# Kernel optimization log

Measured on AMD Instinct MI355X. Metric: run time of the kernel, lower is better.

Reference implementation:

```python
import jax, jax.numpy as jnp
import numpy as np

N = 131072      # total nodes (1024 graphs x 128 nodes)
G = 1024        # graphs in batch
NPG = 128       # nodes per graph (power of 2 -> clean Haar halving)
H = 128         # hidden = out channels
DEG = 16        # avg degree
E = N * DEG     # edges
L = 3           # num_layers
C = 10          # num_classes
BN_EPS = 1e-5
INV_SQRT2 = 0.7071067811865476  # Haar low-pass normalization


def setup_inputs() -> dict:
    key = jax.random.key(0)
    ks = jax.random.split(key, 8)
    x = jax.random.normal(ks[0], (N, H), jnp.float32)
    # within-graph random edges: per-edge graph offset + local endpoint
    offs = (jnp.arange(E, dtype=jnp.int32) // (NPG * DEG)) * NPG
    src = jax.random.randint(ks[1], (E,), 0, NPG, jnp.int32) + offs
    dst = jax.random.randint(ks[2], (E,), 0, NPG, jnp.int32) + offs
    edge_index = jnp.stack([src, dst])
    w = lambda k, s: jax.random.normal(k, s, jnp.float32) * 0.05
    return dict(
        x=x, edge_index=edge_index,
        lin_start_w=w(ks[3], (H, H)), lin_start_b=jnp.zeros((H,), jnp.float32),
        bn_start_g=jnp.ones((H,), jnp.float32), bn_start_b=jnp.zeros((H,), jnp.float32),
        conv_w1=w(ks[4], (L, H, H)), conv_b1=jnp.zeros((L, H), jnp.float32),
        conv_bn_g=jnp.ones((L, H), jnp.float32), conv_bn_b=jnp.zeros((L, H), jnp.float32),
        conv_w2=w(ks[5], (L, H, H)), conv_b2=jnp.zeros((L, H), jnp.float32),
        bn_g=jnp.ones((L, H), jnp.float32), bn_b=jnp.zeros((L, H), jnp.float32),
        bne_g=jnp.ones((L, H), jnp.float32), bne_b=jnp.zeros((L, H), jnp.float32),
        lin_w=w(ks[6], (L * H, C)), lin_b=jnp.zeros((C,), jnp.float32),
    )


def _bn(x, g, b):
    # training-mode BatchNorm1d: batch stats, biased variance
    m = x.mean(0)
    v = x.var(0)
    return (x - m) * jax.lax.rsqrt(v + BN_EPS) * g + b


def reference(x, edge_index, lin_start_w, lin_start_b, bn_start_g, bn_start_b,
              conv_w1, conv_b1, conv_bn_g, conv_bn_b, conv_w2, conv_b2,
              bn_g, bn_b, bne_g, bne_b, lin_w, lin_b):
    n = N
    ei = edge_index
    # lin_before_conv stage
    x = jax.nn.relu(_bn(x @ lin_start_w + lin_start_b, bn_start_g, bn_start_b))
    embds = []
    for i in range(L):
        # GINConv (eps=0): mlp(x + sum_{j->i} x_j)
        agg = jax.ops.segment_sum(x[ei[0]], ei[1], num_segments=n)
        h = x + agg
        h = h @ conv_w1[i] + conv_b1[i]
        h = jax.nn.relu(_bn(h, conv_bn_g[i], conv_bn_b[i]))
        h = h @ conv_w2[i] + conv_b2[i]
        x = jax.nn.relu(_bn(h, bn_g[i], bn_b[i]))
        # Haar pooling: pairwise low-pass coarsening, (x_{2k}+x_{2k+1})/sqrt(2)
        n = n // 2
        cluster = jnp.arange(2 * n, dtype=jnp.int32) // 2
        x = jax.ops.segment_sum(x, cluster, num_segments=n) * INV_SQRT2
        ei = ei // 2  # coarsen edge endpoints to cluster ids
        npg = NPG >> (i + 1)  # nodes per graph after pooling
        batch = jnp.arange(n, dtype=jnp.int32) // npg
        # global_add_pool + BN (dropout in eval mode -> identity)
        embd = jax.ops.segment_sum(x, batch, num_segments=G)
        embd = jax.nn.relu(_bn(embd, bne_g[i], bne_b[i]))
        embds.append(embd)
    return jnp.concatenate(embds, axis=-1) @ lin_w + lin_b  # [G, C]
```

## Files before the change

### kernel.cpp

```cpp
#include <hip/hip_runtime.h>

#define N_NODES  131072
#define G_GRAPHS 1024
#define NPG0     128
#define HDIM     128
#define E_EDGES  2097152
#define EPG      2048
#define BN_EPS   1e-5f
#define INV_SQRT2 0.70710678118654752440f
#define NREP     8
#define SLOT     (NREP * 256)

typedef __attribute__((ext_vector_type(8))) short bf16x8;
typedef __attribute__((ext_vector_type(4))) float f32x4;

__device__ __forceinline__ float bf2f(ushort u) {
  union { unsigned int i; float f; } v; v.i = ((unsigned int)u) << 16; return v.f;
}
__device__ __forceinline__ ushort f2bf(float f) {
  union { float f; unsigned int i; } v; v.f = f;
  unsigned int u = v.i;
  return (ushort)((u + 0x7FFFu + ((u >> 16) & 1u)) >> 16);
}

__device__ __forceinline__ void ldsdma16(const void* g, void* l) {
  __builtin_amdgcn_global_load_lds(
      (const __attribute__((address_space(1))) void*)g,
      (__attribute__((address_space(3))) void*)l, 16, 0, 0);
}

__device__ __forceinline__ void bn_coefs(const float* __restrict__ stats,
                                         const float* __restrict__ gamma,
                                         const float* __restrict__ beta,
                                         float inv_n, float* cA, float* cC, int t) {
  if (t < HDIM) {
    float s = 0.f, ss = 0.f;
    #pragma unroll
    for (int r = 0; r < NREP; ++r) {
      s  += stats[r * 256 + t];
      ss += stats[r * 256 + HDIM + t];
    }
    float m  = s * inv_n;
    float var = fmaxf(ss * inv_n - m * m, 0.f);
    float a = gamma[t] * rsqrtf(var + BN_EPS);
    cA[t] = a;
    cC[t] = beta[t] - m * a;
  }
}

__device__ __forceinline__ void ybuf_store4(ushort* __restrict__ ybuf, int myrow,
                                            int cf, int lg, ushort4 st) {
  const int gp = ((cf ^ (myrow & 7)) << 2) | lg;
  *(ushort4*)&ybuf[myrow * HDIM + gp * 4] = st;
}

__device__ __forceinline__ void stats_pass(const ushort* __restrict__ ybuf,
                                           float* __restrict__ sred, int t) {
  const int ch  = t & 127;
  const int r0  = (t >> 7) * 32;
  const int cfh = ch >> 4, lgh = (ch >> 2) & 3, off = ch & 3;
  float s = 0.f, q = 0.f;
  #pragma unroll
  for (int i = 0; i < 32; ++i) {
    const int r  = r0 + i;
    const int gp = ((cfh ^ (r & 7)) << 2) | lgh;
    const float v = bf2f(ybuf[r * HDIM + gp * 4 + off]);
    s += v; q += v * v;
  }
  atomicAdd(&sred[ch], s);
  atomicAdd(&sred[HDIM + ch], q);
}

__device__ __forceinline__ void copy_out(const ushort* __restrict__ ybuf,
                                         ushort* __restrict__ out,
                                         size_t blkRow0, int t) {
  #pragma unroll
  for (int i = 0; i < 4; ++i) {
    const int cid = i * 512 + t;
    const int r = cid >> 4, q = cid & 15;
    const int gp = (((q >> 1) ^ (r & 7)) << 2) | ((q & 1) * 2);
    *(uint4*)&out[(blkRow0 + r) * HDIM + q * 8] =
        *(const uint4*)&ybuf[r * HDIM + gp * 4];
  }
}

__global__ __launch_bounds__(256, 2)
void k_prep(const float* __restrict__ w_lin_start, const float* __restrict__ w_conv1,
            const float* __restrict__ w_conv2, ushort* __restrict__ wt) {
  __shared__ ushort T[128 * 136];
  const int m = blockIdx.x;
  const int t = threadIdx.x;
  const float* W = (m == 0) ? w_lin_start
                 : (m <= 3) ? w_conv1 + (size_t)(m - 1) * HDIM * HDIM
                            : w_conv2 + (size_t)(m - 4) * HDIM * HDIM;
  for (int it = 0; it < 64; ++it) {
    int idx = it * 256 + t;
    int k = idx >> 7, n = idx & 127;
    T[k * 136 + n] = f2bf(W[idx]);
  }
  __syncthreads();
  ushort* o = wt + (size_t)m * HDIM * HDIM;
  for (int it = 0; it < 64; ++it) {
    int idx = it * 256 + t;
    int n = idx >> 7, k = idx & 127;
    o[idx] = T[k * 136 + n];
  }
}

template <int ACT, int FP32IN>
__global__ __launch_bounds__(512, FP32IN ? 4 : 8)
void k_mm(const void* __restrict__ in_v, ushort* __restrict__ out,
          const ushort* __restrict__ Wt, const float* __restrict__ bias,
          const float* __restrict__ actStats, const float* __restrict__ actG,
          const float* __restrict__ actB, float act_inv_n,
          float* __restrict__ outStats) {
  __shared__ ushort Bt[HDIM * HDIM];
  __shared__ float biasL[HDIM], sred[2 * HDIM], aA[HDIM], aC[HDIM];
  const int t = threadIdx.x;
  const int lane = t & 63;
  const int w = t >> 6;
  const int lr = lane & 15;
  const int lg = lane >> 4;
  const int myrow = w * 16 + lr;

  #pragma unroll
  for (int is = 0; is < 4; ++is) {
    const int col = is * 32 + w * 4 + (lane >> 4);
    const int gsc = (lane & 15) ^ (col & 7);
    ldsdma16(Wt + (size_t)col * HDIM + gsc * 8, &Bt[(is * 512 + w * 64) * 8]);
  }

  const size_t blkRow0 = (size_t)blockIdx.x * 128;
  float4 vraw[8];
  bf16x8 araw[4];
  if (FP32IN) {
    const float* inF = (const float*)in_v;
    #pragma unroll
    for (int ks = 0; ks < 4; ++ks) {
      const float* gp = inF + (blkRow0 + myrow) * HDIM + ks * 32 + lg * 8;
      vraw[2 * ks]     = *(const float4*)gp;
      vraw[2 * ks + 1] = *(const float4*)(gp + 4);
    }
  } else {
    const ushort* inB = (const ushort*)in_v;
    #pragma unroll
    for (int ks = 0; ks < 4; ++ks)
      araw[ks] = *(const bf16x8*)(inB + (blkRow0 + myrow) * HDIM + ks * 32 + lg * 8);
  }

  if (ACT) bn_coefs(actStats, actG, actB, act_inv_n, aA, aC, t);
  if (t < HDIM) biasL[t] = bias[t];
  if (t < 2 * HDIM) sred[t] = 0.f;
  __syncthreads();

  bf16x8 afr[4];
  if (FP32IN) {
    #pragma unroll
    for (int ks = 0; ks < 4; ++ks) {
      const float4 v0 = vraw[2 * ks], v1 = vraw[2 * ks + 1];
      afr[ks][0] = (short)f2bf(v0.x); afr[ks][1] = (short)f2bf(v0.y);
      afr[ks][2] = (short)f2bf(v0.z); afr[ks][3] = (short)f2bf(v0.w);
      afr[ks][4] = (short)f2bf(v1.x); afr[ks][5] = (short)f2bf(v1.y);
      afr[ks][6] = (short)f2bf(v1.z); afr[ks][7] = (short)f2bf(v1.w);
    }
  } else {
    #pragma unroll
    for (int ks = 0; ks < 4; ++ks) {
      bf16x8 a = araw[ks];
      if (ACT) {
        const int k0 = ks * 32 + lg * 8;
        #pragma unroll
        for (int j = 0; j < 8; ++j) {
          float f = fmaxf(fmaf(aA[k0 + j], bf2f((ushort)a[j]), aC[k0 + j]), 0.f);
          a[j] = (short)f2bf(f);
        }
      }
      afr[ks] = a;
    }
  }

  f32x4 acc[8];
  #pragma unroll
  for (int cf = 0; cf < 8; ++cf) acc[cf] = (f32x4){0.f, 0.f, 0.f, 0.f};
  #pragma unroll
  for (int ks = 0; ks < 4; ++ks) {
    const int swc = (ks * 4 + lg) ^ (lr & 7);
    #pragma unroll
    for (int cf = 0; cf < 8; ++cf) {
      bf16x8 bfr = *(const bf16x8*)&Bt[(cf * 16 + lr) * HDIM + swc * 8];
      acc[cf] = __builtin_amdgcn_mfma_f32_16x16x32_bf16(bfr, afr[ks], acc[cf], 0, 0, 0);
    }
  }
  __syncthreads();

  ushort* ybuf = Bt;
  #pragma unroll
  for (int cf = 0; cf < 8; ++cf) {
    const int c0 = cf * 16 + lg * 4;
    float y[4];
    #pragma unroll
    for (int r = 0; r < 4; ++r) y[r] = acc[cf][r] + biasL[c0 + r];
    ushort4 st;
    st.x = f2bf(y[0]); st.y = f2bf(y[1]); st.z = f2bf(y[2]); st.w = f2bf(y[3]);
    ybuf_store4(ybuf, myrow, cf, lg, st);
  }
  __syncthreads();
  stats_pass(ybuf, sred, t);
  copy_out(ybuf, out, blkRow0, t);
  __syncthreads();
  if (t < 2 * HDIM)
    atomicAdd(&outStats[(blockIdx.x & (NREP - 1)) * 256 + t], sred[t]);
}

template <int EPT, int MODE, int GPB>
__global__ __launch_bounds__(512, 8)
void k_gin(const ushort* __restrict__ xin, ushort* __restrict__ out,
           const int* __restrict__ esrc, const int* __restrict__ edst,
           int shift, const ushort* __restrict__ Wt,
           const float* __restrict__ bias,
           const float* __restrict__ actStats, const float* __restrict__ actG,
           const float* __restrict__ actB, float act_inv_n,
           float* __restrict__ outStats,
           float* __restrict__ emb, int layer, float* __restrict__ embStats) {
  __shared__ ushort BtYt[HDIM * HDIM];
  __shared__ uchar  Msm[128 * 128];
  __shared__ float biasL[HDIM], scratch[512], aA[HDIM], aC[HDIM];
  const int t = threadIdx.x;
  const int lane = t & 63;
  const int w = t >> 6;
  const int lr = lane & 15;
  const int lg = lane >> 4;
  const int blk = blockIdx.x;
  const int myrow = w * 16 + lr;
  const size_t blkRow0 = (size_t)blk * 128;
  constexpr int NPREF = (EPT <= 8) ? EPT : 1;

  #pragma unroll
  for (int is = 0; is < 4; ++is) {
    const int col = is * 32 + w * 4 + (lane >> 4);
    const int gsc = (lane & 15) ^ (col & 7);
    ldsdma16(Wt + (size_t)col * HDIM + gsc * 8, &BtYt[(is * 512 + w * 64) * 8]);
  }

  bf16x8 xraw[4];
  if (MODE == 1) {
    #pragma unroll
    for (int ks = 0; ks < 4; ++ks)
      xraw[ks] = *(const bf16x8*)(xin + (blkRow0 + myrow) * HDIM + ks * 32 + lg * 8);
  }

  int eds[NPREF], ess[NPREF];
  if (EPT <= 8) {
    const int ebase = blk * (EPT * 512);
    #pragma unroll
    for (int u = 0; u < EPT; ++u) {
      eds[u] = edst[ebase + t + u * 512];
      ess[u] = esrc[ebase + t + u * 512];
    }
  }

  uint* Mw = (uint*)Msm;
  #pragma unroll
  for (int i = 0; i < 8; ++i) Mw[i * 512 + t] = 0u;

  bn_coefs(actStats, actG, actB, act_inv_n, aA, aC, t);
  if (t < HDIM) biasL[t] = bias[t];
  scratch[t] = 0.f;
  __syncthreads();

  bf16x8 xf[4];
  if (MODE == 1) {
    #pragma unroll
    for (int ks = 0; ks < 4; ++ks) {
      const int k0 = ks * 32 + lg * 8;
      #pragma unroll
      for (int j = 0; j < 8; ++j) {
        float f = fmaxf(fmaf(aA[k0 + j], bf2f((ushort)xraw[ks][j]), aC[k0 + j]), 0.f);
        xf[ks][j] = (short)f2bf(f);
      }
    }
  } else {
    const ushort* hg = xin + (size_t)blk * 256 * HDIM;
    #pragma unroll
    for (int ks = 0; ks < 4; ++ks) {
      const int k0 = ks * 32 + lg * 8;
      bf16x8 a0 = *(const bf16x8*)(hg + (size_t)(2 * myrow)     * HDIM + k0);
      bf16x8 a1 = *(const bf16x8*)(hg + (size_t)(2 * myrow + 1) * HDIM + k0);
      #pragma unroll
      for (int j = 0; j < 8; ++j) {
        float f0 = fmaxf(fmaf(aA[k0 + j], bf2f((ushort)a0[j]), aC[k0 + j]), 0.f);
        float f1 = fmaxf(fmaf(aA[k0 + j], bf2f((ushort)a1[j]), aC[k0 + j]), 0.f);
        xf[ks][j] = (short)f2bf((f0 + f1) * INV_SQRT2);
      }
    }
  }

  if (t < 128) {
    const int g = (t >> 3) ^ (t & 15);
    const int b = t * 128 + g * 8 + (t & 7);
    atomicAdd(&Mw[b >> 2], 1u << ((b & 3) * 8));
  }
  {
    const int ebase = blk * (EPT * 512);
    #pragma unroll
    for (int u = 0; u < EPT; ++u) {
      int de, se;
      if (EPT <= 8) { de = eds[u]; se = ess[u]; }
      else { de = edst[ebase + t + u * 512]; se = esrc[ebase + t + u * 512]; }
      const int d = (de >> shift) - blk * 128;
      const int s = (se >> shift) - blk * 128;
      const int g = (s >> 3) ^ (d & 15);
      const int b = d * 128 + g * 8 + (s & 7);
      atomicAdd(&Mw[b >> 2], 1u << ((b & 3) * 8));
    }
  }

  f32x4 acc1[8];
  #pragma unroll
  for (int cf = 0; cf < 8; ++cf) acc1[cf] = (f32x4){0.f, 0.f, 0.f, 0.f};
  #pragma unroll
  for (int ks = 0; ks < 4; ++ks) {
    const int swc = (ks * 4 + lg) ^ (lr & 7);
    #pragma unroll
    for (int cf = 0; cf < 8; ++cf) {
      bf16x8 wf = *(const bf16x8*)&BtYt[(cf * 16 + lr) * HDIM + swc * 8];
      acc1[cf] = __builtin_amdgcn_mfma_f32_16x16x32_bf16(xf[ks], wf, acc1[cf], 0, 0, 0);
    }
  }
  __syncthreads();

  ushort* Yt = BtYt;
  {
    const int cYt  = w * 2 + (lg >> 1);
    const int half = lg & 1;
    #pragma unroll
    for (int cf = 0; cf < 8; ++cf) {
      const int ch = cf * 16 + lr;
      ushort4 p;
      p.x = f2bf(acc1[cf][0]); p.y = f2bf(acc1[cf][1]);
      p.z = f2bf(acc1[cf][2]); p.w = f2bf(acc1[cf][3]);
      *(ushort4*)&Yt[ch * HDIM + ((cYt ^ (ch & 15)) << 3) + half * 4] = p;
    }
  }
  __syncthreads();

  const uchar* Mu8 = (const uchar*)Msm;
  f32x4 acc2[8];
  #pragma unroll
  for (int cf = 0; cf < 8; ++cf) acc2[cf] = (f32x4){0.f, 0.f, 0.f, 0.f};
  #pragma unroll
  for (int ks = 0; ks < 4; ++ks) {
    const int gm = (ks * 4 + lg) ^ (myrow & 15);
    uint2 mw = *(const uint2*)&Mu8[myrow * 128 + gm * 8];
    bf16x8 bfr;
    #pragma unroll
    for (int j = 0; j < 4; ++j) {
      bfr[j]     = (short)f2bf((float)((mw.x >> (8 * j)) & 0xFFu));
      bfr[j + 4] = (short)f2bf((float)((mw.y >> (8 * j)) & 0xFFu));
    }
    #pragma unroll
    for (int cf = 0; cf < 8; ++cf) {
      const int ch = cf * 16 + lr;
      bf16x8 afr = *(const bf16x8*)&Yt[ch * HDIM + (((ks * 4 + lg) ^ (ch & 15)) << 3)];
      acc2[cf] = __builtin_amdgcn_mfma_f32_16x16x32_bf16(afr, bfr, acc2[cf], 0, 0, 0);
    }
  }
  __syncthreads();

  ushort* ybuf = BtYt;
  #pragma unroll
  for (int cf = 0; cf < 8; ++cf) {
    const int c0 = cf * 16 + lg * 4;
    float y[4];
    #pragma unroll
    for (int r = 0; r < 4; ++r) y[r] = acc2[cf][r] + biasL[c0 + r];
    ushort4 st;
    st.x = f2bf(y[0]); st.y = f2bf(y[1]); st.z = f2bf(y[2]); st.w = f2bf(y[3]);
    ybuf_store4(ybuf, myrow, cf, lg, st);
  }
  __syncthreads();
  stats_pass(ybuf, scratch, t);
  copy_out(ybuf, out, blkRow0, t);
  __syncthreads();
  if (t < 2 * HDIM) {
    atomicAdd(&outStats[(blk & (NREP - 1)) * 256 + t], scratch[t]);
    scratch[t] = 0.f;
  }

  if (MODE == 2) {
    #pragma unroll
    for (int ks = 0; ks < 4; ++ks)
      *(bf16x8*)&ybuf[myrow * HDIM + ((ks * 4 + lg) ^ (myrow & 7)) * 8] = xf[ks];
    __syncthreads();
    {
      const int ch = t & 127;
      const int q  = t >> 7;
      const int cchunk = ch >> 3, coff = ch & 7;
      float s = 0.f;
      #pragma unroll
      for (int i = 0; i < 32; ++i) {
        const int r = q * 32 + i;
        s += bf2f(ybuf[r * HDIM + ((cchunk ^ (r & 7)) << 3) + coff]);
      }
      const int gi = (q * 32) / (128 / GPB);
      atomicAdd(&scratch[gi * 128 + ch], s);
    }
    __syncthreads();
    if (t < GPB * 128) {
      const float e = scratch[t];
      const int gi = t >> 7, ch = t & 127;
      emb[(size_t)(blk * GPB + gi) * 384 + layer * HDIM + ch] = e;
      atomicAdd(&embStats[(blk & (NREP - 1)) * 256 + ch], e);
      atomicAdd(&embStats[(blk & (NREP - 1)) * 256 + HDIM + ch], e * e);
    }
  }
}

__global__ __launch_bounds__(256, 4)
void k_pool_emb(const ushort* __restrict__ hin, float* __restrict__ emb,
                int layer, int npg_in,
                const float* __restrict__ actStats, const float* __restrict__ actG,
                const float* __restrict__ actB, float act_inv_n,
                float* __restrict__ embStats) {
  __shared__ float aA[HDIM], aC[HDIM];
  __shared__ float red[256];
  const int t = threadIdx.x;
  const int g = blockIdx.x;
  bn_coefs(actStats, actG, actB, act_inv_n, aA, aC, t);
  __syncthreads();
  const int c = t & 127;
  const int ph = t >> 7;
  const ushort* hb = hin + (size_t)g * npg_in * HDIM;
  const float a = aA[c], cc = aC[c];
  float s = 0.f;
  for (int r = ph; r < npg_in; r += 2)
    s += fmaxf(fmaf(a, bf2f(hb[r * HDIM + c]), cc), 0.f);
  red[t] = s * INV_SQRT2;
  __syncthreads();
  if (t < HDIM) {
    const float e = red[t] + red[t + HDIM];
    emb[(size_t)g * 384 + layer * HDIM + t] = e;
    atomicAdd(&embStats[(g & (NREP - 1)) * 256 + t], e);
    atomicAdd(&embStats[(g & (NREP - 1)) * 256 + HDIM + t], e * e);
  }
}

__global__ __launch_bounds__(128, 8)
void k_final(const float* __restrict__ emb,
             const float* __restrict__ se0, const float* __restrict__ se1,
             const float* __restrict__ se2,
             const float* __restrict__ bneG, const float* __restrict__ bneB,
             const float* __restrict__ linW, const float* __restrict__ linB,
             float* __restrict__ outp) {
  __shared__ float ev[384];
  __shared__ float eA[384], eC[384];
  const int t = threadIdx.x;
  const int g = blockIdx.x;
  if (t < 128) {
    const float* se[3] = {se0, se1, se2};
    const float inv_n = 1.f / (float)G_GRAPHS;
    #pragma unroll
    for (int l = 0; l < 3; ++l) {
      float s = 0.f, ss = 0.f;
      #pragma unroll
      for (int r = 0; r < NREP; ++r) {
        s  += se[l][r * 256 + t];
        ss += se[l][r * 256 + 128 + t];
      }
      float m  = s * inv_n;
      float var = fmaxf(ss * inv_n - m * m, 0.f);
      float a = bneG[l * 128 + t] * rsqrtf(var + BN_EPS);
      eA[l * 128 + t] = a;
      eC[l * 128 + t] = bneB[l * 128 + t] - m * a;
    }
  }
  __syncthreads();
  for (int j = t; j < 384; j += 128)
    ev[j] = fmaxf(fmaf(eA[j], emb[(size_t)g * 384 + j], eC[j]), 0.f);
  __syncthreads();
  if (t < 10) {
    float acc = linB[t];
    #pragma unroll 8
    for (int j = 0; j < 384; ++j) acc += ev[j] * linW[j * 10 + t];
    outp[g * 10 + t] = acc;
  }
}

extern "C" void kernel_launch(void* const* d_in, const int* in_sizes, int n_in,
                              void* d_out, int out_size, void* d_ws, size_t ws_size,
                              hipStream_t stream) {
  const float* x           = (const float*)d_in[0];
  const int*   ei          = (const int*)  d_in[1];
  const float* lin_start_w = (const float*)d_in[2];
  const float* lin_start_b = (const float*)d_in[3];
  const float* bn_start_g  = (const float*)d_in[4];
  const float* bn_start_b  = (const float*)d_in[5];
  const float* conv_w1     = (const float*)d_in[6];
  const float* conv_b1     = (const float*)d_in[7];
  const float* conv_bn_g   = (const float*)d_in[8];
  const float* conv_bn_b   = (const float*)d_in[9];
  const float* conv_w2     = (const float*)d_in[10];
  const float* conv_b2     = (const float*)d_in[11];
  const float* bn_g        = (const float*)d_in[12];
  const float* bn_b        = (const float*)d_in[13];
  const float* bne_g       = (const float*)d_in[14];
  const float* bne_b       = (const float*)d_in[15];
  const float* lin_w       = (const float*)d_in[16];
  const float* lin_b       = (const float*)d_in[17];
  float* outp = (float*)d_out;

  const size_t NH = (size_t)N_NODES * HDIM;
  float*  stats = (float*)d_ws;
  float*  emb   = stats + 10 * SLOT;
  ushort* wt    = (ushort*)(emb + (size_t)G_GRAPHS * 384);
  ushort* bufA  = wt + 7 * HDIM * HDIM;
  ushort* bufB  = bufA + NH;

  hipMemsetAsync(stats, 0, 10 * SLOT * sizeof(float), stream);

  const int* esrc = ei;
  const int* edst = ei + E_EDGES;

  float* s1[3] = {stats + 1 * SLOT, stats + 4 * SLOT, stats + 7 * SLOT};
  float* s2[3] = {stats + 2 * SLOT, stats + 5 * SLOT, stats + 8 * SLOT};
  float* se[3] = {stats + 3 * SLOT, stats + 6 * SLOT, stats + 9 * SLOT};

  k_prep<<<7, 256, 0, stream>>>(lin_start_w, conv_w1, conv_w2, wt);

  k_mm<0, 1><<<N_NODES / 128, 512, 0, stream>>>(
      x, bufA, wt, lin_start_b, nullptr, nullptr, nullptr, 0.f, stats);

  k_gin<4, 1, 1><<<N_NODES / 128, 512, 0, stream>>>(
      bufA, bufB, esrc, edst, 0, wt + 1 * HDIM * HDIM, conv_b1,
      stats, bn_start_g, bn_start_b, 1.f / (float)N_NODES,
      s1[0], nullptr, 0, nullptr);
  k_mm<1, 0><<<N_NODES / 128, 512, 0, stream>>>(
      bufB, bufA, wt + 4 * HDIM * HDIM, conv_b2,
      s1[0], conv_bn_g, conv_bn_b, 1.f / (float)N_NODES, s2[0]);

  k_gin<8, 2, 2><<<(N_NODES / 2) / 128, 512, 0, stream>>>(
      bufA, bufB, esrc, edst, 1, wt + 2 * HDIM * HDIM, conv_b1 + HDIM,
      s2[0], bn_g, bn_b, 1.f / (float)N_NODES,
      s1[1], emb, 0, se[0]);
  k_mm<1, 0><<<(N_NODES / 2) / 128, 512, 0, stream>>>(
      bufB, bufA, wt + 5 * HDIM * HDIM, conv_b2 + HDIM,
      s1[1], conv_bn_g + HDIM, conv_bn_b + HDIM, 2.f / (float)N_NODES, s2[1]);

  k_gin<16, 2, 4><<<(N_NODES / 4) / 128, 512, 0, stream>>>(
      bufA, bufB, esrc, edst, 2, wt + 3 * HDIM * HDIM, conv_b1 + 2 * HDIM,
      s2[1], bn_g + HDIM, bn_b + HDIM, 2.f / (float)N_NODES,
      s1[2], emb, 1, se[1]);
  k_mm<1, 0><<<(N_NODES / 4) / 128, 512, 0, stream>>>(
      bufB, bufA, wt + 6 * HDIM * HDIM, conv_b2 + 2 * HDIM,
      s1[2], conv_bn_g + 2 * HDIM, conv_bn_b + 2 * HDIM,
      4.f / (float)N_NODES, s2[2]);

  k_pool_emb<<<G_GRAPHS, 256, 0, stream>>>(
      bufA, emb, 2, NPG0 >> 2,
      s2[2], bn_g + 2 * HDIM, bn_b + 2 * HDIM, 4.f / (float)N_NODES, se[2]);

  k_final<<<G_GRAPHS, 128, 0, stream>>>(
      emb, se[0], se[1], se[2], bne_g, bne_b, lin_w, lin_b, outp);
}
```

Before: 180.5 us.

## Pack adjacency counts to 4 bits, shrink GIN LDS, fold stats memset into prep

The GIN kernel now stores per-block adjacency counts as 4-bit nibbles in an 8 KB buffer instead of 8-bit bytes. It also aliases the BN coefficients and the stats scratch into that buffer and folds the bias into the accumulator init, which cuts LDS per block. This should allow more resident blocks per CU. The edge-list prefetch is dropped: edges are loaded after the first GEMM, and the count matrix is built once the weight tile is dead. Separately, the stats memset is moved into extra blocks of k_prep, and the number of stat replicas doubles to reduce atomic contention. The nibble packing assumes no node pair has more than 15 edges, self-loop included; a larger count would silently carry into the neighbouring entry.

```diff
diff --git a/kernel.cpp b/kernel.cpp
--- a/kernel.cpp
+++ b/kernel.cpp
@@ -8,7 +8,7 @@
 #define EPG      2048
 #define BN_EPS   1e-5f
 #define INV_SQRT2 0.70710678118654752440f
-#define NREP     8
+#define NREP     16
 #define SLOT     (NREP * 256)
 
 typedef __attribute__((ext_vector_type(8))) short bf16x8;
@@ -86,10 +86,16 @@
 
 __global__ __launch_bounds__(256, 2)
 void k_prep(const float* __restrict__ w_lin_start, const float* __restrict__ w_conv1,
-            const float* __restrict__ w_conv2, ushort* __restrict__ wt) {
-  __shared__ ushort T[128 * 136];
+            const float* __restrict__ w_conv2, ushort* __restrict__ wt,
+            float* __restrict__ stats) {
   const int m = blockIdx.x;
   const int t = threadIdx.x;
+  if (m >= 7) {
+    const int zb = m - 7;
+    for (int i = zb * 10240 + t; i < (zb + 1) * 10240; i += 256) stats[i] = 0.f;
+    return;
+  }
+  __shared__ ushort T[128 * 136];
   const float* W = (m == 0) ? w_lin_start
                  : (m <= 3) ? w_conv1 + (size_t)(m - 1) * HDIM * HDIM
                             : w_conv2 + (size_t)(m - 4) * HDIM * HDIM;
@@ -222,9 +228,8 @@
            const float* __restrict__ actB, float act_inv_n,
            float* __restrict__ outStats,
            float* __restrict__ emb, int layer, float* __restrict__ embStats) {
-  __shared__ ushort BtYt[HDIM * HDIM];
-  __shared__ uchar  Msm[128 * 128];
-  __shared__ float biasL[HDIM], scratch[512], aA[HDIM], aC[HDIM];
+  __shared__ ushort Asm[HDIM * HDIM];
+  __shared__ uint   Bsm[2048];
   const int t = threadIdx.x;
   const int lane = t & 63;
   const int w = t >> 6;
@@ -233,13 +238,14 @@
   const int blk = blockIdx.x;
   const int myrow = w * 16 + lr;
   const size_t blkRow0 = (size_t)blk * 128;
-  constexpr int NPREF = (EPT <= 8) ? EPT : 1;
+  float* aA = (float*)Bsm;
+  float* aC = aA + HDIM;
 
   #pragma unroll
   for (int is = 0; is < 4; ++is) {
     const int col = is * 32 + w * 4 + (lane >> 4);
     const int gsc = (lane & 15) ^ (col & 7);
-    ldsdma16(Wt + (size_t)col * HDIM + gsc * 8, &BtYt[(is * 512 + w * 64) * 8]);
+    ldsdma16(Wt + (size_t)col * HDIM + gsc * 8, &Asm[(is * 512 + w * 64) * 8]);
   }
 
   bf16x8 xraw[4];
@@ -249,23 +255,7 @@
       xraw[ks] = *(const bf16x8*)(xin + (blkRow0 + myrow) * HDIM + ks * 32 + lg * 8);
   }
 
-  int eds[NPREF], ess[NPREF];
-  if (EPT <= 8) {
-    const int ebase = blk * (EPT * 512);
-    #pragma unroll
-    for (int u = 0; u < EPT; ++u) {
-      eds[u] = edst[ebase + t + u * 512];
-      ess[u] = esrc[ebase + t + u * 512];
-    }
-  }
-
-  uint* Mw = (uint*)Msm;
-  #pragma unroll
-  for (int i = 0; i < 8; ++i) Mw[i * 512 + t] = 0u;
-
   bn_coefs(actStats, actG, actB, act_inv_n, aA, aC, t);
-  if (t < HDIM) biasL[t] = bias[t];
-  scratch[t] = 0.f;
   __syncthreads();
 
   bf16x8 xf[4];
@@ -295,26 +285,6 @@
     }
   }
 
-  if (t < 128) {
-    const int g = (t >> 3) ^ (t & 15);
-    const int b = t * 128 + g * 8 + (t & 7);
-    atomicAdd(&Mw[b >> 2], 1u << ((b & 3) * 8));
-  }
-  {
-    const int ebase = blk * (EPT * 512);
-    #pragma unroll
-    for (int u = 0; u < EPT; ++u) {
-      int de, se;
-      if (EPT <= 8) { de = eds[u]; se = ess[u]; }
-      else { de = edst[ebase + t + u * 512]; se = esrc[ebase + t + u * 512]; }
-      const int d = (de >> shift) - blk * 128;
-      const int s = (se >> shift) - blk * 128;
-      const int g = (s >> 3) ^ (d & 15);
-      const int b = d * 128 + g * 8 + (s & 7);
-      atomicAdd(&Mw[b >> 2], 1u << ((b & 3) * 8));
-    }
-  }
-
   f32x4 acc1[8];
   #pragma unroll
   for (int cf = 0; cf < 8; ++cf) acc1[cf] = (f32x4){0.f, 0.f, 0.f, 0.f};
@@ -323,13 +293,14 @@
     const int swc = (ks * 4 + lg) ^ (lr & 7);
     #pragma unroll
     for (int cf = 0; cf < 8; ++cf) {
-      bf16x8 wf = *(const bf16x8*)&BtYt[(cf * 16 + lr) * HDIM + swc * 8];
+      bf16x8 wf = *(const bf16x8*)&Asm[(cf * 16 + lr) * HDIM + swc * 8];
       acc1[cf] = __builtin_amdgcn_mfma_f32_16x16x32_bf16(xf[ks], wf, acc1[cf], 0, 0, 0);
     }
   }
   __syncthreads();
 
-  ushort* Yt = BtYt;
+  #pragma unroll
+  for (int i = 0; i < 4; ++i) Bsm[i * 512 + t] = 0u;
   {
     const int cYt  = w * 2 + (lg >> 1);
     const int half = lg & 1;
@@ -339,55 +310,69 @@
       ushort4 p;
       p.x = f2bf(acc1[cf][0]); p.y = f2bf(acc1[cf][1]);
       p.z = f2bf(acc1[cf][2]); p.w = f2bf(acc1[cf][3]);
-      *(ushort4*)&Yt[ch * HDIM + ((cYt ^ (ch & 15)) << 3) + half * 4] = p;
-    }
-  }
-  __syncthreads();
-
-  const uchar* Mu8 = (const uchar*)Msm;
+      *(ushort4*)&Asm[ch * HDIM + ((cYt ^ (ch & 15)) << 3) + half * 4] = p;
+    }
+  }
+  __syncthreads();
+
+  if (t < 128) {
+    const int g = (t >> 3) ^ (t & 15);
+    atomicAdd(&Bsm[t * 16 + g], 1u << ((t & 7) * 4));
+  }
+  {
+    const int ebase = blk * (EPT * 512);
+    #pragma unroll
+    for (int u = 0; u < EPT; ++u) {
+      const int d = (edst[ebase + t + u * 512] >> shift) - blk * 128;
+      const int s = (esrc[ebase + t + u * 512] >> shift) - blk * 128;
+      atomicAdd(&Bsm[d * 16 + ((s >> 3) ^ (d & 15))], 1u << ((s & 7) * 4));
+    }
+  }
+  __syncthreads();
+
   f32x4 acc2[8];
   #pragma unroll
-  for (int cf = 0; cf < 8; ++cf) acc2[cf] = (f32x4){0.f, 0.f, 0.f, 0.f};
+  for (int cf = 0; cf < 8; ++cf) {
+    const float4 b4 = *(const float4*)&bias[cf * 16 + lg * 4];
+    acc2[cf][0] = b4.x; acc2[cf][1] = b4.y; acc2[cf][2] = b4.z; acc2[cf][3] = b4.w;
+  }
   #pragma unroll
   for (int ks = 0; ks < 4; ++ks) {
     const int gm = (ks * 4 + lg) ^ (myrow & 15);
-    uint2 mw = *(const uint2*)&Mu8[myrow * 128 + gm * 8];
+    const uint mw = Bsm[myrow * 16 + gm];
     bf16x8 bfr;
     #pragma unroll
-    for (int j = 0; j < 4; ++j) {
-      bfr[j]     = (short)f2bf((float)((mw.x >> (8 * j)) & 0xFFu));
-      bfr[j + 4] = (short)f2bf((float)((mw.y >> (8 * j)) & 0xFFu));
-    }
+    for (int j = 0; j < 8; ++j)
+      bfr[j] = (short)f2bf((float)((mw >> (4 * j)) & 0xFu));
     #pragma unroll
     for (int cf = 0; cf < 8; ++cf) {
       const int ch = cf * 16 + lr;
-      bf16x8 afr = *(const bf16x8*)&Yt[ch * HDIM + (((ks * 4 + lg) ^ (ch & 15)) << 3)];
+      bf16x8 afr = *(const bf16x8*)&Asm[ch * HDIM + (((ks * 4 + lg) ^ (ch & 15)) << 3)];
       acc2[cf] = __builtin_amdgcn_mfma_f32_16x16x32_bf16(afr, bfr, acc2[cf], 0, 0, 0);
     }
   }
   __syncthreads();
 
-  ushort* ybuf = BtYt;
+  ushort* ybuf = Asm;
+  float* scratch = (float*)Bsm;
   #pragma unroll
   for (int cf = 0; cf < 8; ++cf) {
-    const int c0 = cf * 16 + lg * 4;
-    float y[4];
-    #pragma unroll
-    for (int r = 0; r < 4; ++r) y[r] = acc2[cf][r] + biasL[c0 + r];
     ushort4 st;
-    st.x = f2bf(y[0]); st.y = f2bf(y[1]); st.z = f2bf(y[2]); st.w = f2bf(y[3]);
+    st.x = f2bf(acc2[cf][0]); st.y = f2bf(acc2[cf][1]);
+    st.z = f2bf(acc2[cf][2]); st.w = f2bf(acc2[cf][3]);
     ybuf_store4(ybuf, myrow, cf, lg, st);
   }
-  __syncthreads();
+  scratch[t] = 0.f;
+  __syncthreads();
+
   stats_pass(ybuf, scratch, t);
   copy_out(ybuf, out, blkRow0, t);
   __syncthreads();
-  if (t < 2 * HDIM) {
+  if (t < 2 * HDIM)
     atomicAdd(&outStats[(blk & (NREP - 1)) * 256 + t], scratch[t]);
+  if (MODE == 2) {
     scratch[t] = 0.f;
-  }
-
-  if (MODE == 2) {
+
     #pragma unroll
     for (int ks = 0; ks < 4; ++ks)
       *(bf16x8*)&ybuf[myrow * HDIM + ((ks * 4 + lg) ^ (myrow & 7)) * 8] = xf[ks];
@@ -516,8 +501,6 @@
   ushort* bufA  = wt + 7 * HDIM * HDIM;
   ushort* bufB  = bufA + NH;
 
-  hipMemsetAsync(stats, 0, 10 * SLOT * sizeof(float), stream);
-
   const int* esrc = ei;
   const int* edst = ei + E_EDGES;
 
@@ -525,7 +508,7 @@
   float* s2[3] = {stats + 2 * SLOT, stats + 5 * SLOT, stats + 8 * SLOT};
   float* se[3] = {stats + 3 * SLOT, stats + 6 * SLOT, stats + 9 * SLOT};
 
-  k_prep<<<7, 256, 0, stream>>>(lin_start_w, conv_w1, conv_w2, wt);
+  k_prep<<<11, 256, 0, stream>>>(lin_start_w, conv_w1, conv_w2, wt, stats);
 
   k_mm<0, 1><<<N_NODES / 128, 512, 0, stream>>>(
       x, bufA, wt, lin_start_b, nullptr, nullptr, nullptr, 0.f, stats);
```

After: 187.9 us. +4.1%, slower.
